# Optimization experiments

Measured on AMD Instinct MI355X. Metric: run time of the kernel, lower is better.

## Reference

```python
import jax, jax.numpy as jnp
import numpy as np

THR = 0.2
POOL_A = 160
POOL_B = 96
EPS = 1e-5


def _adaptive_avg_pool_last(x, out_size):
    # torch AdaptiveAvgPool1d semantics: bin i averages [floor(i*n/o), ceil((i+1)*n/o))
    n = x.shape[-1]
    i = np.arange(out_size)
    starts = (i * n) // out_size
    ends = -((-(i + 1) * n) // out_size)
    cs = jnp.cumsum(x, axis=-1)
    cs = jnp.concatenate([jnp.zeros_like(cs[..., :1]), cs], axis=-1)
    sums = cs[..., ends] - cs[..., starts]
    return sums / jnp.asarray(ends - starts, x.dtype)


def _unfold3x3(x, H, W):
    # Faithful to torch: raw reshape (N, L, C) -> (N, C, H, W) (memory reinterpretation,
    # NOT a transpose), then F.unfold(k=3, pad=1) and rearrange 'n (c ww) l -> n l ww c'.
    N, L, C = x.shape
    img = x.reshape(N, C, H, W)
    pad = jnp.pad(img, ((0, 0), (0, 0), (1, 1), (1, 1)))
    # window positions in row-major (ky, kx) order, matching F.unfold
    patches = jnp.stack([pad[:, :, dy:dy + H, dx:dx + W]
                         for dy in range(3) for dx in range(3)], axis=2)  # (N,C,9,H,W)
    return patches.transpose(0, 3, 4, 2, 1).reshape(N, H * W, 9, C)  # (N,L,9,C)


def _forward(feat_s0, feat_s1, ln_weight, ln_bias):
    N, L, C = feat_s0.shape
    H = W = int(round(L ** 0.5))
    conf = jnp.einsum('nlc,nsc->nls', feat_s0, feat_s1) / (C ** 0.5)
    conf = jax.nn.softmax(conf, axis=1) * jax.nn.softmax(conf, axis=2)
    # mutual nearest-neighbor mask with confidence threshold
    mask = ((conf > THR)
            & (conf == conf.max(axis=2, keepdims=True))
            & (conf == conf.max(axis=1, keepdims=True))).astype(feat_s0.dtype)
    u0 = _unfold3x3(feat_s0, H, W)
    u1 = _unfold3x3(feat_s1, H, W)
    sem0 = jnp.einsum('nlc,nlwc->nlw', feat_s0, u0) / C  # divided by C (shape[-1]), as in source
    sem1 = jnp.einsum('nlc,nlwc->nlw', feat_s1, u1) / C
    fea0 = jnp.einsum('nlwc,nlw->nlc', u0, sem0)
    fea1 = jnp.einsum('nlwc,nlw->nlc', u1, sem1)
    s0 = jnp.einsum('nls,nsd->nld', mask, fea1) / L
    s1 = jnp.einsum('nsl,nsd->nld', mask, fea0) / L
    f0 = jnp.concatenate([_adaptive_avg_pool_last(feat_s0, POOL_A),
                          _adaptive_avg_pool_last(s0, POOL_B)], axis=-1)
    f1 = jnp.concatenate([_adaptive_avg_pool_last(feat_s1, POOL_A),
                          _adaptive_avg_pool_last(s1, POOL_B)], axis=-1)
    f = jnp.concatenate([f0, f1], axis=0)  # (2N, L, 256)
    mu = f.mean(-1, keepdims=True)
    var = f.var(-1, keepdims=True)
    f = (f - mu) * jax.lax.rsqrt(var + EPS) * ln_weight + ln_bias
    return f[:N], f[N:]


def setup_inputs():
    key = jax.random.key(0)
    k0, k1 = jax.random.split(key)
    N, L, C = 2, 4096, 256
    return {
        'feat_s0': jax.random.normal(k0, (N, L, C), jnp.float32),
        'feat_s1': jax.random.normal(k1, (N, L, C), jnp.float32),
        'ln_weight': jnp.ones((C,), jnp.float32),
        'ln_bias': jnp.zeros((C,), jnp.float32),
    }


def reference(feat_s0, feat_s1, ln_weight, ln_bias):
    return _forward(feat_s0, feat_s1, ln_weight, ln_bias)
```

## Files before the change

### kernel.cpp

```cpp
#include <hip/hip_runtime.h>
#include <stdint.h>

#define NBATCH 2
#define LL 4096
#define CC 256
#define LSTR 68
#define KEXP 0.09016844f
#define KEXP2 0.18033688f
#define IMIN (-2147483647 - 1)

typedef short bf16x8 __attribute__((ext_vector_type(8)));
typedef float f32x4 __attribute__((ext_vector_type(4)));

__device__ __forceinline__ uint16_t f2bf(float f){
  union { float f; uint32_t u; } v; v.f = f;
  return (uint16_t)((v.u + 0x7fffu + ((v.u >> 16) & 1u)) >> 16);
}

__global__ __launch_bounds__(256) void cast_bf16(
    const float* __restrict__ a, const float* __restrict__ b,
    uint16_t* __restrict__ oa, uint16_t* __restrict__ ob){
  int idx = blockIdx.x * 256 + threadIdx.x;
  float4 va = ((const float4*)a)[idx];
  float4 vb = ((const float4*)b)[idx];
  ushort4 ua, ub;
  ua.x = f2bf(va.x); ua.y = f2bf(va.y); ua.z = f2bf(va.z); ua.w = f2bf(va.w);
  ub.x = f2bf(vb.x); ub.y = f2bf(vb.y); ub.z = f2bf(vb.z); ub.w = f2bf(vb.w);
  ((ushort4*)oa)[idx] = ua;
  ((ushort4*)ob)[idx] = ub;
}

__global__ __launch_bounds__(256) void conf_pass(
    const uint16_t* __restrict__ f0b, const uint16_t* __restrict__ f1b,
    float* __restrict__ rowSum, float* __restrict__ colSum,
    int* __restrict__ rowPart, int* __restrict__ colPart){
  __shared__ uint16_t Alds[128*LSTR], Blds[128*LSTR];
  __shared__ float rowS[2][128], colS[2][128];
  __shared__ int rb[128][2], cb[128][2];
  int st = blockIdx.x, lt = blockIdx.y, n = blockIdx.z;
  int t = threadIdx.x;
  const int wv = t >> 6, lane = t & 63, lr = lane & 15, quad = lane >> 4;
  const int lq = wv >> 1, sq = wv & 1;
  const uint16_t* A = f0b + (size_t)n*LL*CC;
  const uint16_t* B = f1b + (size_t)n*LL*CC;
  f32x4 acc[4][4];
  #pragma unroll
  for (int r = 0; r < 4; r++)
    #pragma unroll
    for (int j = 0; j < 4; j++) acc[r][j] = (f32x4){0.f,0.f,0.f,0.f};
  for (int kc = 0; kc < 4; kc++){
    __syncthreads();
    #pragma unroll
    for (int m = 0; m < 4; m++){
      int f = m*256 + t, row = f >> 3, kg = f & 7;
      *(float4*)(Alds + row*LSTR + kg*8) =
          *(const float4*)(A + (size_t)(lt*128 + row)*CC + kc*64 + kg*8);
      *(float4*)(Blds + row*LSTR + kg*8) =
          *(const float4*)(B + (size_t)(st*128 + row)*CC + kc*64 + kg*8);
    }
    __syncthreads();
    #pragma unroll
    for (int kk = 0; kk < 2; kk++){
      bf16x8 a[4], b[4];
      #pragma unroll
      for (int r = 0; r < 4; r++)
        a[r] = *(const bf16x8*)(Alds + (lq*64 + r*16 + lr)*LSTR + kk*32 + quad*8);
      #pragma unroll
      for (int j = 0; j < 4; j++)
        b[j] = *(const bf16x8*)(Blds + (sq*64 + j*16 + lr)*LSTR + kk*32 + quad*8);
      #pragma unroll
      for (int r = 0; r < 4; r++)
        #pragma unroll
        for (int j = 0; j < 4; j++)
          acc[r][j] = __builtin_amdgcn_mfma_f32_16x16x32_bf16(a[r], b[j], acc[r][j], 0, 0, 0);
    }
  }
  const int sbase = st*128 + sq*64 + lr;
  const int lbase = lt*128 + lq*64 + quad*4;
  float rsum[4][4], csum[4] = {0.f,0.f,0.f,0.f};
  int rkey[4][4], ckey[4] = {IMIN,IMIN,IMIN,IMIN};
  #pragma unroll
  for (int r = 0; r < 4; r++)
    #pragma unroll
    for (int rr = 0; rr < 4; rr++){ rsum[r][rr] = 0.f; rkey[r][rr] = IMIN; }
  #pragma unroll
  for (int r = 0; r < 4; r++)
    #pragma unroll
    for (int j = 0; j < 4; j++)
      #pragma unroll
      for (int rr = 0; rr < 4; rr++){
        float a = acc[r][j][rr];
        float e = exp2f(a * KEXP);
        rsum[r][rr] += e;
        csum[j] += e;
        int iqs = ((int)(a * 2048.f)) << 12;
        int sk = iqs + (sbase + j*16);
        int lk = iqs + (lbase + r*16 + rr);
        rkey[r][rr] = max(rkey[r][rr], sk);
        ckey[j] = max(ckey[j], lk);
      }
  #pragma unroll
  for (int msk = 1; msk <= 8; msk <<= 1)
    #pragma unroll
    for (int r = 0; r < 4; r++)
      #pragma unroll
      for (int rr = 0; rr < 4; rr++){
        rsum[r][rr] += __shfl_xor(rsum[r][rr], msk);
        rkey[r][rr] = max(rkey[r][rr], __shfl_xor(rkey[r][rr], msk));
      }
  #pragma unroll
  for (int msk = 16; msk <= 32; msk <<= 1)
    #pragma unroll
    for (int j = 0; j < 4; j++){
      csum[j] += __shfl_xor(csum[j], msk);
      ckey[j] = max(ckey[j], __shfl_xor(ckey[j], msk));
    }
  if (lr == 0){
    #pragma unroll
    for (int r = 0; r < 4; r++)
      #pragma unroll
      for (int rr = 0; rr < 4; rr++){
        int row = lq*64 + r*16 + quad*4 + rr;
        rowS[sq][row] = rsum[r][rr];
        rb[row][sq]   = rkey[r][rr];
      }
  }
  if (quad == 0){
    #pragma unroll
    for (int j = 0; j < 4; j++){
      int col = sq*64 + j*16 + lr;
      colS[lq][col] = csum[j];
      cb[col][lq]   = ckey[j];
    }
  }
  __syncthreads();
  if (t < 128){
    rowSum[((size_t)n*LL + lt*128 + t)*32 + st] = rowS[0][t] + rowS[1][t];
    colSum[((size_t)n*LL + st*128 + t)*32 + lt] = colS[0][t] + colS[1][t];
    rowPart[((size_t)n*LL + lt*128 + t)*32 + st] = max(rb[t][0], rb[t][1]);
    colPart[((size_t)n*LL + st*128 + t)*32 + lt] = max(cb[t][0], cb[t][1]);
  }
}

__global__ __launch_bounds__(256) void reduce_all(
    const float* __restrict__ rowSum, const float* __restrict__ colSum,
    const int* __restrict__ rowPart, const int* __restrict__ colPart,
    float* __restrict__ R, float* __restrict__ Cv,
    int* __restrict__ rowKI, int* __restrict__ colKI){
  int row = blockIdx.x * 4 + (threadIdx.x >> 6);
  int lane = threadIdx.x & 63;
  int side = blockIdx.y;
  const float* sums = side ? colSum  : rowSum;
  const int*   part = side ? colPart : rowPart;
  float s = 0.f; int k = IMIN;
  if (lane < 32){
    s = sums[(size_t)row*32 + lane];
    k = part[(size_t)row*32 + lane];
  }
  #pragma unroll
  for (int msk = 1; msk <= 32; msk <<= 1){
    s += __shfl_xor(s, msk);
    k = max(k, __shfl_xor(k, msk));
  }
  if (lane == 0){
    if (side){ Cv[row] = s; colKI[row] = k; }
    else     { R [row] = s; rowKI[row] = k; }
  }
}

__device__ float fea_fly(const float* __restrict__ featn, int srow, int t){
  __shared__ float sred[9][4];
  __shared__ float ssem[9];
  int lane = t & 63, wv = t >> 6;
  int h = srow >> 6, xx = srow & 63;
  float fv = featn[(size_t)srow * CC + t];
  float uv[9];
  #pragma unroll
  for (int w = 0; w < 9; w++){
    int dy = w/3 - 1, dx = w%3 - 1;
    int y = h + dy, x = xx + dx;
    uv[w] = (y >= 0 && y < 64 && x >= 0 && x < 64) ? featn[(size_t)t * 4096 + y*64 + x] : 0.f;
  }
  __syncthreads();
  #pragma unroll
  for (int w = 0; w < 9; w++){
    float pvv = fv * uv[w];
    #pragma unroll
    for (int msk = 1; msk <= 32; msk <<= 1) pvv += __shfl_xor(pvv, msk);
    if (lane == 0) sred[w][wv] = pvv;
  }
  __syncthreads();
  if (t < 9) ssem[t] = (sred[t][0] + sred[t][1] + sred[t][2] + sred[t][3]) * (1.f/256.f);
  __syncthreads();
  float acc = 0.f;
  #pragma unroll
  for (int w = 0; w < 9; w++) acc += uv[w] * ssem[w];
  __syncthreads();
  return acc;
}

__device__ __forceinline__ float pool_window(const float* f, const float* s, int t){
  if (t < 160){
    int a = (t*8)/5, e = (t*8+12)/5;
    float sum = 0.f;
    for (int i = a; i < e; i++) sum += f[i];
    return sum / (float)(e - a);
  } else {
    int tt = t - 160;
    int a = (tt*8)/3, e = (tt*8+10)/3;
    float sum = 0.f;
    for (int i = a; i < e; i++) sum += s[i];
    return sum / (float)(e - a);
  }
}

__global__ __launch_bounds__(256) void tail(
    const float* __restrict__ feat0, const float* __restrict__ feat1,
    const float* __restrict__ R, const float* __restrict__ Cv,
    const int* __restrict__ rowKI, const int* __restrict__ colKI,
    const float* __restrict__ lnw, const float* __restrict__ lnb,
    float* __restrict__ out){
  int l = blockIdx.x, n = blockIdx.y, t = threadIdx.x;
  size_t base = (size_t)n * LL;
  float v0 = 0.f, v1 = 0.f;
  {
    int kr = rowKI[base + l];
    int ss = kr & 4095;
    float araw = (float)(kr >> 12) * (1.f/2048.f);
    float val = exp2f(araw * KEXP2) / (R[base + l] * Cv[base + ss]);
    if (val > 0.2f && (colKI[base + ss] & 4095) == l)
      v0 = fea_fly(feat1 + (size_t)n*LL*CC, ss, t) * (1.f/4096.f);
  }
  {
    int kc = colKI[base + l];
    int ss = kc & 4095;
    float araw = (float)(kc >> 12) * (1.f/2048.f);
    float val = exp2f(araw * KEXP2) / (Cv[base + l] * R[base + ss]);
    if (val > 0.2f && (rowKI[base + ss] & 4095) == l)
      v1 = fea_fly(feat0 + (size_t)n*LL*CC, ss, t) * (1.f/4096.f);
  }
  __shared__ float f0r[CC], f1r[CC], s0r[CC], s1r[CC];
  __shared__ float redA[2][4], redB[2][4];
  f0r[t] = feat0[(base + l)*CC + t];
  f1r[t] = feat1[(base + l)*CC + t];
  s0r[t] = v0;
  s1r[t] = v1;
  __syncthreads();
  float pA = pool_window(f0r, s0r, t);
  float pB = pool_window(f1r, s1r, t);
  float smA = pA, sqA = pA*pA, smB = pB, sqB = pB*pB;
  #pragma unroll
  for (int msk = 1; msk <= 32; msk <<= 1){
    smA += __shfl_xor(smA, msk);
    sqA += __shfl_xor(sqA, msk);
    smB += __shfl_xor(smB, msk);
    sqB += __shfl_xor(sqB, msk);
  }
  int lane = t & 63, wv = t >> 6;
  if (lane == 0){ redA[0][wv] = smA; redA[1][wv] = sqA; redB[0][wv] = smB; redB[1][wv] = sqB; }
  __syncthreads();
  float tsA = redA[0][0]+redA[0][1]+redA[0][2]+redA[0][3];
  float tqA = redA[1][0]+redA[1][1]+redA[1][2]+redA[1][3];
  float tsB = redB[0][0]+redB[0][1]+redB[0][2]+redB[0][3];
  float tqB = redB[1][0]+redB[1][1]+redB[1][2]+redB[1][3];
  float muA = tsA * (1.f/256.f), varA = tqA * (1.f/256.f) - muA*muA;
  float muB = tsB * (1.f/256.f), varB = tqB * (1.f/256.f) - muB*muB;
  float w = lnw[t], bsh = lnb[t];
  out[((size_t)n*LL + l)*CC + t]       = (pA - muA) * rsqrtf(varA + 1e-5f) * w + bsh;
  out[((size_t)(2 + n)*LL + l)*CC + t] = (pB - muB) * rsqrtf(varB + 1e-5f) * w + bsh;
}

extern "C" void kernel_launch(void* const* d_in, const int* in_sizes, int n_in,
                              void* d_out, int out_size, void* d_ws, size_t ws_size,
                              hipStream_t stream){
  const float* feat0 = (const float*)d_in[0];
  const float* feat1 = (const float*)d_in[1];
  const float* lnw   = (const float*)d_in[2];
  const float* lnb   = (const float*)d_in[3];
  float* out = (float*)d_out;
  char* ws = (char*)d_ws;
  const size_t MB = 1024 * 1024;
  uint16_t* f0b = (uint16_t*)(ws + 0);
  uint16_t* f1b = (uint16_t*)(ws + 4*MB);
  float* R     = (float*)(ws + 8*MB);
  float* Cv    = (float*)(ws + 8*MB + 32*1024);
  int*   rowKI = (int*)  (ws + 8*MB + 64*1024);
  int*   colKI = (int*)  (ws + 8*MB + 96*1024);
  float* rowSum = (float*)(ws + 9*MB);
  float* colSum = (float*)(ws + 10*MB);
  int*   rowPart = (int*) (ws + 11*MB);
  int*   colPart = (int*) (ws + 12*MB);

  cast_bf16<<<2048, 256, 0, stream>>>(feat0, feat1, f0b, f1b);
  dim3 gconf(32, 32, NBATCH);
  conf_pass<<<gconf, 256, 0, stream>>>(f0b, f1b, rowSum, colSum, rowPart, colPart);
  dim3 gred(NBATCH*LL/4, 2);
  reduce_all<<<gred, 256, 0, stream>>>(rowSum, colSum, rowPart, colPart,
                                       R, Cv, rowKI, colKI);
  dim3 gt(LL, NBATCH);
  tail<<<gt, 256, 0, stream>>>(feat0, feat1, R, Cv, rowKI, colKI, lnw, lnb, out);
}
```

Measured before the change: 139.3 us.

## Fuse row/col reductions into conf_pass via atomics and load A directly from global

```diff
diff --git a/kernel.cpp b/kernel.cpp
--- a/kernel.cpp
+++ b/kernel.cpp
@@ -32,9 +32,9 @@
 
 __global__ __launch_bounds__(256) void conf_pass(
     const uint16_t* __restrict__ f0b, const uint16_t* __restrict__ f1b,
-    float* __restrict__ rowSum, float* __restrict__ colSum,
-    int* __restrict__ rowPart, int* __restrict__ colPart){
-  __shared__ uint16_t Alds[128*LSTR], Blds[128*LSTR];
+    float* __restrict__ R, float* __restrict__ Cv,
+    uint32_t* __restrict__ rowKI, uint32_t* __restrict__ colKI){
+  __shared__ uint16_t Blds[128*LSTR];
   __shared__ float rowS[2][128], colS[2][128];
   __shared__ int rb[128][2], cb[128][2];
   int st = blockIdx.x, lt = blockIdx.y, n = blockIdx.z;
@@ -43,6 +43,10 @@
   const int lq = wv >> 1, sq = wv & 1;
   const uint16_t* A = f0b + (size_t)n*LL*CC;
   const uint16_t* B = f1b + (size_t)n*LL*CC;
+  const uint16_t* arow[4];
+  #pragma unroll
+  for (int r = 0; r < 4; r++)
+    arow[r] = A + (size_t)(lt*128 + lq*64 + r*16 + lr)*CC + quad*8;
   f32x4 acc[4][4];
   #pragma unroll
   for (int r = 0; r < 4; r++)
@@ -53,8 +57,6 @@
     #pragma unroll
     for (int m = 0; m < 4; m++){
       int f = m*256 + t, row = f >> 3, kg = f & 7;
-      *(float4*)(Alds + row*LSTR + kg*8) =
-          *(const float4*)(A + (size_t)(lt*128 + row)*CC + kc*64 + kg*8);
       *(float4*)(Blds + row*LSTR + kg*8) =
           *(const float4*)(B + (size_t)(st*128 + row)*CC + kc*64 + kg*8);
     }
@@ -64,7 +66,7 @@
       bf16x8 a[4], b[4];
       #pragma unroll
       for (int r = 0; r < 4; r++)
-        a[r] = *(const bf16x8*)(Alds + (lq*64 + r*16 + lr)*LSTR + kk*32 + quad*8);
+        a[r] = *(const bf16x8*)(arow[r] + kc*64 + kk*32);
       #pragma unroll
       for (int j = 0; j < 4; j++)
         b[j] = *(const bf16x8*)(Blds + (sq*64 + j*16 + lr)*LSTR + kk*32 + quad*8);
@@ -94,10 +96,8 @@
         rsum[r][rr] += e;
         csum[j] += e;
         int iqs = ((int)(a * 2048.f)) << 12;
-        int sk = iqs + (sbase + j*16);
-        int lk = iqs + (lbase + r*16 + rr);
-        rkey[r][rr] = max(rkey[r][rr], sk);
-        ckey[j] = max(ckey[j], lk);
+        rkey[r][rr] = max(rkey[r][rr], iqs + (sbase + j*16));
+        ckey[j]     = max(ckey[j],     iqs + (lbase + r*16 + rr));
       }
   #pragma unroll
   for (int msk = 1; msk <= 8; msk <<= 1)
@@ -135,36 +135,12 @@
   }
   __syncthreads();
   if (t < 128){
-    rowSum[((size_t)n*LL + lt*128 + t)*32 + st] = rowS[0][t] + rowS[1][t];
-    colSum[((size_t)n*LL + st*128 + t)*32 + lt] = colS[0][t] + colS[1][t];
-    rowPart[((size_t)n*LL + lt*128 + t)*32 + st] = max(rb[t][0], rb[t][1]);
-    colPart[((size_t)n*LL + st*128 + t)*32 + lt] = max(cb[t][0], cb[t][1]);
-  }
-}
-
-__global__ __launch_bounds__(256) void reduce_all(
-    const float* __restrict__ rowSum, const float* __restrict__ colSum,
-    const int* __restrict__ rowPart, const int* __restrict__ colPart,
-    float* __restrict__ R, float* __restrict__ Cv,
-    int* __restrict__ rowKI, int* __restrict__ colKI){
-  int row = blockIdx.x * 4 + (threadIdx.x >> 6);
-  int lane = threadIdx.x & 63;
-  int side = blockIdx.y;
-  const float* sums = side ? colSum  : rowSum;
-  const int*   part = side ? colPart : rowPart;
-  float s = 0.f; int k = IMIN;
-  if (lane < 32){
-    s = sums[(size_t)row*32 + lane];
-    k = part[(size_t)row*32 + lane];
-  }
-  #pragma unroll
-  for (int msk = 1; msk <= 32; msk <<= 1){
-    s += __shfl_xor(s, msk);
-    k = max(k, __shfl_xor(k, msk));
-  }
-  if (lane == 0){
-    if (side){ Cv[row] = s; colKI[row] = k; }
-    else     { R [row] = s; rowKI[row] = k; }
+    atomicAdd(&R [(size_t)n*LL + lt*128 + t], rowS[0][t] + rowS[1][t]);
+    atomicAdd(&Cv[(size_t)n*LL + st*128 + t], colS[0][t] + colS[1][t]);
+    atomicMax(&rowKI[(size_t)n*LL + lt*128 + t],
+              (uint32_t)max(rb[t][0], rb[t][1]) ^ 0x80000000u);
+    atomicMax(&colKI[(size_t)n*LL + st*128 + t],
+              (uint32_t)max(cb[t][0], cb[t][1]) ^ 0x80000000u);
   }
 }
 
@@ -217,26 +193,26 @@
 __global__ __launch_bounds__(256) void tail(
     const float* __restrict__ feat0, const float* __restrict__ feat1,
     const float* __restrict__ R, const float* __restrict__ Cv,
-    const int* __restrict__ rowKI, const int* __restrict__ colKI,
+    const uint32_t* __restrict__ rowKI, const uint32_t* __restrict__ colKI,
     const float* __restrict__ lnw, const float* __restrict__ lnb,
     float* __restrict__ out){
   int l = blockIdx.x, n = blockIdx.y, t = threadIdx.x;
   size_t base = (size_t)n * LL;
   float v0 = 0.f, v1 = 0.f;
   {
-    int kr = rowKI[base + l];
+    int kr = (int)(rowKI[base + l] ^ 0x80000000u);
     int ss = kr & 4095;
     float araw = (float)(kr >> 12) * (1.f/2048.f);
     float val = exp2f(araw * KEXP2) / (R[base + l] * Cv[base + ss]);
-    if (val > 0.2f && (colKI[base + ss] & 4095) == l)
+    if (val > 0.2f && (int)((colKI[base + ss] ^ 0x80000000u) & 4095u) == l)
       v0 = fea_fly(feat1 + (size_t)n*LL*CC, ss, t) * (1.f/4096.f);
   }
   {
-    int kc = colKI[base + l];
+    int kc = (int)(colKI[base + l] ^ 0x80000000u);
     int ss = kc & 4095;
     float araw = (float)(kc >> 12) * (1.f/2048.f);
     float val = exp2f(araw * KEXP2) / (Cv[base + l] * R[base + ss]);
-    if (val > 0.2f && (rowKI[base + ss] & 4095) == l)
+    if (val > 0.2f && (int)((rowKI[base + ss] ^ 0x80000000u) & 4095u) == l)
       v1 = fea_fly(feat0 + (size_t)n*LL*CC, ss, t) * (1.f/4096.f);
   }
   __shared__ float f0r[CC], f1r[CC], s0r[CC], s1r[CC];
@@ -282,21 +258,15 @@
   const size_t MB = 1024 * 1024;
   uint16_t* f0b = (uint16_t*)(ws + 0);
   uint16_t* f1b = (uint16_t*)(ws + 4*MB);
-  float* R     = (float*)(ws + 8*MB);
-  float* Cv    = (float*)(ws + 8*MB + 32*1024);
-  int*   rowKI = (int*)  (ws + 8*MB + 64*1024);
-  int*   colKI = (int*)  (ws + 8*MB + 96*1024);
-  float* rowSum = (float*)(ws + 9*MB);
-  float* colSum = (float*)(ws + 10*MB);
-  int*   rowPart = (int*) (ws + 11*MB);
-  int*   colPart = (int*) (ws + 12*MB);
+  float*    R     = (float*)   (ws + 8*MB);
+  float*    Cv    = (float*)   (ws + 8*MB + 32*1024);
+  uint32_t* rowKI = (uint32_t*)(ws + 8*MB + 64*1024);
+  uint32_t* colKI = (uint32_t*)(ws + 8*MB + 96*1024);
 
   cast_bf16<<<2048, 256, 0, stream>>>(feat0, feat1, f0b, f1b);
+  hipMemsetAsync(ws + 8*MB, 0, 128*1024, stream);
   dim3 gconf(32, 32, NBATCH);
-  conf_pass<<<gconf, 256, 0, stream>>>(f0b, f1b, rowSum, colSum, rowPart, colPart);
-  dim3 gred(NBATCH*LL/4, 2);
-  reduce_all<<<gred, 256, 0, stream>>>(rowSum, colSum, rowPart, colPart,
-                                       R, Cv, rowKI, colKI);
+  conf_pass<<<gconf, 256, 0, stream>>>(f0b, f1b, R, Cv, rowKI, colKI);
   dim3 gt(LL, NBATCH);
   tail<<<gt, 256, 0, stream>>>(feat0, feat1, R, Cv, rowKI, colKI, lnw, lnb, out);
 }
```

New measurement: 149.3 us. 1.07x slower.
